# Performance work log

Hardware: AMD Instinct MI355X
Metric: run time of the kernel (lower is better)

## Reference

```python
import jax, jax.numpy as jnp
import numpy as np

B, A = 1024, 256                 # batch, padded action-space size
N_ENT, N_REL = 100000, 500
E_DIM, R_DIM, H_DIM = 200, 200, 400
ACT_DIM = E_DIM + R_DIM          # action embedding = [rel_emb ; ent_emb]
IN_DIM = E_DIM + H_DIM + R_DIM   # X = cat([E, H, Q])
HUGE = 1e31                      # ops.HUGE_INT
EPS = 1e-20


def setup_inputs() -> dict:
    key = jax.random.key(0)
    ks = jax.random.split(key, 12)
    inp = {
        "e": jax.random.randint(ks[0], (B,), 0, N_ENT),
        "q": jax.random.randint(ks[1], (B,), 0, N_REL),
        "H": jax.random.normal(ks[2], (B, H_DIM), dtype=jnp.float32),
        "r_space": jax.random.randint(ks[3], (B, A), 0, N_REL),
        "e_space": jax.random.randint(ks[4], (B, A), 0, N_ENT),
        "action_mask": jax.random.randint(ks[5], (B, A), 0, 2).astype(jnp.int32),
        # learned parameters
        "entity_emb": jax.random.normal(ks[6], (N_ENT, E_DIM), dtype=jnp.float32) * 0.02,
        "relation_emb": jax.random.normal(ks[7], (N_REL, R_DIM), dtype=jnp.float32) * 0.02,
        "W1": jax.random.normal(ks[8], (IN_DIM, ACT_DIM), dtype=jnp.float32) * (1.0 / np.sqrt(IN_DIM)),
        "b1": jnp.zeros((ACT_DIM,), jnp.float32),
        "W2": jax.random.normal(ks[9], (ACT_DIM, ACT_DIM), dtype=jnp.float32) * (1.0 / np.sqrt(ACT_DIM)),
        "b2": jnp.zeros((ACT_DIM,), jnp.float32),
        "W_att": jax.random.normal(ks[10], (ACT_DIM, R_DIM), dtype=jnp.float32) * (1.0 / np.sqrt(ACT_DIM)),
        "b_att": jnp.zeros((R_DIM,), jnp.float32),
    }
    return inp


def reference(e, q, H, r_space, e_space, action_mask,
              entity_emb, relation_emb, W1, b1, W2, b2, W_att, b_att):
    # state featurization: X = cat([E, H, Q])  -> [B, IN_DIM]
    E = entity_emb[e]
    Q = relation_emb[q]
    X = jnp.concatenate([E, H, Q], axis=-1)
    X = jax.nn.relu(X @ W1 + b1)          # W1 + ReLU (dropout = identity in eval)
    X2 = X @ W2 + b2                      # [B, ACT_DIM]

    # relation attention over all relations
    relation_att = jax.nn.softmax((X2 @ W_att + b_att) @ relation_emb.T, axis=-1)  # [B, N_REL]

    # action embeddings: A = cat([rel_emb[r_space], ent_emb[e_space]])  [B, A, ACT_DIM]
    A_emb = jnp.concatenate([relation_emb[r_space], entity_emb[e_space]], axis=-1)

    mask = action_mask.astype(X2.dtype)
    scores = jnp.einsum('bad,bd->ba', A_emb, X2) - (1.0 - mask) * HUGE
    action_dist = jax.nn.softmax(scores, axis=-1)                      # [B, A]
    entropy = -jnp.sum(action_dist * jnp.log(action_dist + EPS), axis=-1)  # [B]
    return action_dist, entropy, relation_att
```

## Files before the change

kernel.cpp:

```cpp
#include <hip/hip_runtime.h>

#define BATCH   1024
#define ASZ     256
#define EDIM    200
#define RDIM    200
#define HDIM    400
#define ACTDIM  400
#define INDIM   800
#define NRELS   500

typedef __attribute__((ext_vector_type(8))) short short8v;
typedef __attribute__((ext_vector_type(4))) float float4v;
typedef unsigned short u16;

__device__ __forceinline__ u16 f2bf(float f) {
    union { float f; unsigned u; } v; v.f = f;
    unsigned r = v.u + 0x7FFFu + ((v.u >> 16) & 1u);
    return (u16)(r >> 16);
}

template<int ABF, int BBF, int CT, int GAT, int RELU>
__device__ __forceinline__ void mgemm_body(
    const void* __restrict__ A, const void* __restrict__ B,
    float* __restrict__ Cp, u16* __restrict__ CTout, int ldct,
    const float* __restrict__ bias, float* __restrict__ Cf, u16* __restrict__ Cb,
    int M, int N, int K, int bn, int bm, int z, int nz,
    const int* e_s, const int* q_s,
    const float* __restrict__ Hm, const float* __restrict__ ent,
    const float* __restrict__ rel,
    short* As, short* Bs, int t)
{
    const int tot = (K + 31) >> 5;
    const int s0 = (z * tot) / nz, s1 = ((z + 1) * tot) / nz;

    const int lane = t & 63, w = t >> 6;
    const int l15 = lane & 15, l4 = lane >> 4;
    const int wr = (w >> 1) * 32, wc = (w & 1) * 32;

    const int row = t >> 2;
    const int kc  = (t & 3) * 8;

    auto loadA = [&](int s) -> uint4 {
        const int gk = (s << 5) + kc;
        __attribute__((aligned(16))) u16 v[8];
        if (GAT) {
            const float* p;
            if (gk < EDIM)              p = ent + (long)e_s[row] * EDIM + gk;
            else if (gk < EDIM + HDIM)  p = Hm  + (long)(bm + row) * HDIM + (gk - EDIM);
            else                        p = rel + (long)q_s[row] * RDIM + (gk - EDIM - HDIM);
            float4 f0 = *(const float4*)p;
            float4 f1 = *(const float4*)(p + 4);
            v[0]=f2bf(f0.x); v[1]=f2bf(f0.y); v[2]=f2bf(f0.z); v[3]=f2bf(f0.w);
            v[4]=f2bf(f1.x); v[5]=f2bf(f1.y); v[6]=f2bf(f1.z); v[7]=f2bf(f1.w);
            return *(uint4*)v;
        }
        const int gr = bm + row;
        if (gr < M && gk + 8 <= K) {
            if (ABF) return *(const uint4*)((const u16*)A + (long)gr * K + gk);
            const float* p = (const float*)A + (long)gr * K + gk;
            float4 f0 = *(const float4*)p;
            float4 f1 = *(const float4*)(p + 4);
            v[0]=f2bf(f0.x); v[1]=f2bf(f0.y); v[2]=f2bf(f0.z); v[3]=f2bf(f0.w);
            v[4]=f2bf(f1.x); v[5]=f2bf(f1.y); v[6]=f2bf(f1.z); v[7]=f2bf(f1.w);
            return *(uint4*)v;
        }
#pragma unroll
        for (int i = 0; i < 8; ++i) v[i] = 0;
        return *(uint4*)v;
    };
    auto loadB = [&](int s) -> uint4 {
        const int gk = (s << 5) + kc;
        const int gr = bn + row;
        __attribute__((aligned(16))) u16 v[8];
        if (gr < N && gk + 8 <= K) {
            if (BBF) return *(const uint4*)((const u16*)B + (long)gr * K + gk);
            const float* p = (const float*)B + (long)gr * K + gk;
            float4 f0 = *(const float4*)p;
            float4 f1 = *(const float4*)(p + 4);
            v[0]=f2bf(f0.x); v[1]=f2bf(f0.y); v[2]=f2bf(f0.z); v[3]=f2bf(f0.w);
            v[4]=f2bf(f1.x); v[5]=f2bf(f1.y); v[6]=f2bf(f1.z); v[7]=f2bf(f1.w);
            return *(uint4*)v;
        }
#pragma unroll
        for (int i = 0; i < 8; ++i) v[i] = 0;
        return *(uint4*)v;
    };

    float4v acc00 = {0.f,0.f,0.f,0.f}, acc01 = {0.f,0.f,0.f,0.f};
    float4v acc10 = {0.f,0.f,0.f,0.f}, acc11 = {0.f,0.f,0.f,0.f};

    uint4 ra = loadA(s0);
    uint4 rb = loadB(s0);

    for (int s = s0; s < s1; ++s) {
        *(uint4*)&As[row * 40 + kc] = ra;
        *(uint4*)&Bs[row * 40 + kc] = rb;
        __syncthreads();
        if (s + 1 < s1) {
            ra = loadA(s + 1);
            rb = loadB(s + 1);
        }
        short8v a0 = *(short8v*)&As[(wr      + l15) * 40 + l4 * 8];
        short8v a1 = *(short8v*)&As[(wr + 16 + l15) * 40 + l4 * 8];
        short8v b0 = *(short8v*)&Bs[(wc      + l15) * 40 + l4 * 8];
        short8v b1 = *(short8v*)&Bs[(wc + 16 + l15) * 40 + l4 * 8];
        acc00 = __builtin_amdgcn_mfma_f32_16x16x32_bf16(a0, b0, acc00, 0, 0, 0);
        acc01 = __builtin_amdgcn_mfma_f32_16x16x32_bf16(a0, b1, acc01, 0, 0, 0);
        acc10 = __builtin_amdgcn_mfma_f32_16x16x32_bf16(a1, b0, acc10, 0, 0, 0);
        acc11 = __builtin_amdgcn_mfma_f32_16x16x32_bf16(a1, b1, acc11, 0, 0, 0);
        __syncthreads();
    }

    const int rm0 = bm + wr + l4 * 4;
    const int cn0 = bn + wc + l15;
    if (CT == 1) {
        float* dst = Cp + (long)z * M * N;
#pragma unroll
        for (int r = 0; r < 4; ++r) {
            int gm0 = rm0 + r, gm1 = rm0 + 16 + r;
            if (gm0 < M) {
                if (cn0 < N)      dst[(long)gm0 * N + cn0]      = acc00[r];
                if (cn0 + 16 < N) dst[(long)gm0 * N + cn0 + 16] = acc01[r];
            }
            if (gm1 < M) {
                if (cn0 < N)      dst[(long)gm1 * N + cn0]      = acc10[r];
                if (cn0 + 16 < N) dst[(long)gm1 * N + cn0 + 16] = acc11[r];
            }
        }
    } else if (CT == 2) {
#pragma unroll
        for (int r = 0; r < 4; ++r) {
            int gm0 = rm0 + r, gm1 = rm0 + 16 + r;
            if (gm0 < M) {
                if (cn0 < N)      CTout[(long)cn0 * ldct + gm0]        = f2bf(acc00[r]);
                if (cn0 + 16 < N) CTout[(long)(cn0 + 16) * ldct + gm0] = f2bf(acc01[r]);
            }
            if (gm1 < M) {
                if (cn0 < N)      CTout[(long)cn0 * ldct + gm1]        = f2bf(acc10[r]);
                if (cn0 + 16 < N) CTout[(long)(cn0 + 16) * ldct + gm1] = f2bf(acc11[r]);
            }
        }
    } else {
        float bv0 = (cn0 < N)      ? bias[cn0]      : 0.f;
        float bv1 = (cn0 + 16 < N) ? bias[cn0 + 16] : 0.f;
#pragma unroll
        for (int r = 0; r < 4; ++r) {
            int gm0 = rm0 + r, gm1 = rm0 + 16 + r;
            if (gm0 < M) {
                if (cn0 < N) {
                    float v = acc00[r] + bv0;
                    if (RELU) v = fmaxf(v, 0.f);
                    Cf[(long)gm0 * N + cn0] = v;
                    Cb[(long)gm0 * N + cn0] = f2bf(v);
                }
                if (cn0 + 16 < N) {
                    float v = acc01[r] + bv1;
                    if (RELU) v = fmaxf(v, 0.f);
                    Cf[(long)gm0 * N + cn0 + 16] = v;
                    Cb[(long)gm0 * N + cn0 + 16] = f2bf(v);
                }
            }
            if (gm1 < M) {
                if (cn0 < N) {
                    float v = acc10[r] + bv0;
                    if (RELU) v = fmaxf(v, 0.f);
                    Cf[(long)gm1 * N + cn0] = v;
                    Cb[(long)gm1 * N + cn0] = f2bf(v);
                }
                if (cn0 + 16 < N) {
                    float v = acc11[r] + bv1;
                    if (RELU) v = fmaxf(v, 0.f);
                    Cf[(long)gm1 * N + cn0 + 16] = v;
                    Cb[(long)gm1 * N + cn0 + 16] = f2bf(v);
                }
            }
        }
    }
}

template<int ABF, int BBF, int CT, int GAT, int RELU>
__global__ __launch_bounds__(256) void k_mgemm(
    const void* __restrict__ A, const void* __restrict__ B,
    float* __restrict__ Cp, u16* __restrict__ CTout, int ldct,
    const float* __restrict__ bias, float* __restrict__ Cf, u16* __restrict__ Cb,
    int M, int N, int K,
    const int* __restrict__ eidx, const int* __restrict__ qidx,
    const float* __restrict__ Hm, const float* __restrict__ ent,
    const float* __restrict__ rel)
{
    __shared__ __align__(16) short As[64 * 40];
    __shared__ __align__(16) short Bs[64 * 40];
    __shared__ int e_s[64], q_s[64];
    const int t = threadIdx.x;
    const int bm = blockIdx.y * 64;
    if (GAT) {
        if (t < 64) {
            e_s[t] = eidx[bm + t];
            q_s[t] = qidx[bm + t];
        }
        __syncthreads();
    }
    mgemm_body<ABF, BBF, CT, GAT, RELU>(A, B, Cp, CTout, ldct, bias, Cf, Cb,
                                        M, N, K, blockIdx.x * 64, bm,
                                        blockIdx.z, gridDim.z,
                                        e_s, q_s, Hm, ent, rel, As, Bs, t);
}

__global__ __launch_bounds__(256) void k_prep_all(
    const float* __restrict__ W1, const float* __restrict__ W2,
    const float* __restrict__ batt, const float* __restrict__ rel,
    const float* __restrict__ Watt,
    u16* __restrict__ W1t, u16* __restrict__ W2t,
    u16* __restrict__ BbigT, float* __restrict__ bbig2)
{
    __shared__ __align__(16) short As[64 * 40];
    __shared__ __align__(16) short Bs[64 * 40];
    __shared__ float tile[32][33];
    __shared__ float bs[200];

    int blk = blockIdx.x, t = threadIdx.x;

    if (blk < 325) {
        int tk = blk / 13, tn = blk % 13;
        int k0 = tk * 32, n0 = tn * 32;
        int i = t >> 3, j4 = (t & 7) * 4;
#pragma unroll
        for (int jj = 0; jj < 4; ++jj) {
            int n = n0 + j4 + jj;
            tile[i][j4 + jj] = (n < 400) ? W1[(long)(k0 + i) * 400 + n] : 0.f;
        }
        __syncthreads();
        int o = t >> 3;
        if (n0 + o < 400) {
            ushort4 u;
            u.x = f2bf(tile[j4 + 0][o]); u.y = f2bf(tile[j4 + 1][o]);
            u.z = f2bf(tile[j4 + 2][o]); u.w = f2bf(tile[j4 + 3][o]);
            *(ushort4*)(W1t + (long)(n0 + o) * 800 + k0 + j4) = u;
        }
    } else if (blk < 494) {
        int idx = blk - 325;
        int tk = idx / 13, tn = idx % 13;
        int k0 = tk * 32, n0 = tn * 32;
        int i = t >> 3, j4 = (t & 7) * 4;
#pragma unroll
        for (int jj = 0; jj < 4; ++jj) {
            int n = n0 + j4 + jj;
            tile[i][j4 + jj] = (k0 + i < 400 && n < 400) ? W2[(long)(k0 + i) * 400 + n] : 0.f;
        }
        __syncthreads();
        int o = t >> 3;
        if (n0 + o < 400) {
#pragma unroll
            for (int jj = 0; jj < 4; ++jj) {
                int k = k0 + j4 + jj;
                if (k < 400) W2t[(long)(n0 + o) * 400 + k] = f2bf(tile[j4 + jj][o]);
            }
        }
    } else if (blk < 594) {
        int gid = (blk - 494) * 256 + t;
        for (int g = gid; g < 50000; g += 100 * 256) {
            int n = g / 100, kq = (g % 100) * 4;
            ushort4 u;
            u.x = (kq + 0 < 200) ? f2bf(rel[(long)n * 200 + kq + 0]) : (u16)0;
            u.y = (kq + 1 < 200) ? f2bf(rel[(long)n * 200 + kq + 1]) : (u16)0;
            u.z = (kq + 2 < 200) ? f2bf(rel[(long)n * 200 + kq + 2]) : (u16)0;
            u.w = (kq + 3 < 200) ? f2bf(rel[(long)n * 200 + kq + 3]) : (u16)0;
            *(ushort4*)(BbigT + (long)(500 + n) * 400 + kq) = u;
        }
    } else if (blk == 594) {
        if (t < 200) bs[t] = batt[t];
        __syncthreads();
        for (int n = t; n < NRELS; n += 256) {
            const float* rr = rel + (long)n * RDIM;
            float s = 0.f;
            for (int k = 0; k < 200; ++k) s += bs[k] * rr[k];
            bbig2[n] = s;
        }
    } else {
        int idx = blk - 595;
        int bn = (idx & 7) * 64, bm = (idx >> 3) * 64;
        mgemm_body<0, 0, 2, 0, 0>(Watt, rel, nullptr, BbigT, 400,
                                  nullptr, nullptr, nullptr,
                                  400, 500, 200, bn, bm, 0, 1,
                                  nullptr, nullptr, nullptr, nullptr, nullptr,
                                  As, Bs, t);
    }
}

template<int RELU, int OUT>
__global__ __launch_bounds__(128) void k_reduce2(
    const float* __restrict__ Cp, const float* __restrict__ bias,
    float* __restrict__ Cf, u16* __restrict__ Cb, int M, int N, int nks)
{
    int m = blockIdx.x;
    int nf4 = N >> 2;
    for (int f = threadIdx.x; f < nf4; f += 128) {
        long off = (long)m * N + f * 4;
        float4 s = *(const float4*)(Cp + off);
        for (int ks = 1; ks < nks; ++ks) {
            float4 v = *(const float4*)(Cp + (long)ks * M * N + off);
            s.x += v.x; s.y += v.y; s.z += v.z; s.w += v.w;
        }
        float4 bb = *(const float4*)(bias + f * 4);
        s.x += bb.x; s.y += bb.y; s.z += bb.z; s.w += bb.w;
        if (RELU) {
            s.x = fmaxf(s.x, 0.f); s.y = fmaxf(s.y, 0.f);
            s.z = fmaxf(s.z, 0.f); s.w = fmaxf(s.w, 0.f);
        }
        if (OUT != 1) *(float4*)(Cf + off) = s;
        if (OUT != 0) {
            ushort4 u;
            u.x = f2bf(s.x); u.y = f2bf(s.y); u.z = f2bf(s.z); u.w = f2bf(s.w);
            *(ushort4*)(Cb + off) = u;
        }
    }
}

__global__ __launch_bounds__(512) void k_scores(
    const float* __restrict__ X2, const float* __restrict__ Cp,
    const float* __restrict__ brel,
    const int* __restrict__ r_space, const int* __restrict__ e_space,
    const int* __restrict__ amask,
    const float* __restrict__ ent_emb,
    float* __restrict__ out_dist, float* __restrict__ out_ent,
    float* __restrict__ out_rel)
{
    int b = blockIdx.x, t = threadIdx.x;
    int wave = t >> 6, lane = t & 63;
    __shared__ __align__(16) float4 xt4[50];
    __shared__ float xr[NRELS];
    __shared__ float sc[ASZ];
    __shared__ int   smask[ASZ];
    __shared__ float red[8];

    const float* rowX2 = X2 + (long)b * ACTDIM;
    const float* c0 = Cp + (long)b * 1000;
    const float* c1 = Cp + (long)BATCH * 1000 + (long)b * 1000;
    if (t < 50) xt4[t] = *(const float4*)(rowX2 + 200 + 4 * t);
    for (int i = t; i < NRELS; i += 512) xr[i] = c0[500 + i] + c1[500 + i];

    int abase = wave * 32;
    int r_idx = 0, e_idx = 0, mk = 0;
    if (lane < 32) {
        long base = (long)b * ASZ + abase + lane;
        r_idx = r_space[base];
        e_idx = e_space[base];
        mk    = amask[base];
        smask[abase + lane] = mk;
    }
    __syncthreads();

    float4 x = (lane < 50) ? xt4[lane] : make_float4(0.f, 0.f, 0.f, 0.f);
    const int g = lane >> 4;

#pragma unroll
    for (int i = 0; i < 4; ++i) {
        float s[8] = {0.f,0.f,0.f,0.f,0.f,0.f,0.f,0.f};
        int rj[8];
#pragma unroll
        for (int j = 0; j < 8; ++j) {
            int a = 8 * i + j;
            int m0 = __shfl(mk, a);
            rj[j]  = __shfl(r_idx, a);
            if (m0) {
                int e0 = __shfl(e_idx, a);
                if (lane < 50) {
                    float4 v = ((const float4*)(ent_emb + (long)e0 * EDIM))[lane];
                    s[j] = fmaf(v.x, x.x, fmaf(v.y, x.y, fmaf(v.z, x.z, v.w * x.w)));
                }
            }
        }
#pragma unroll
        for (int j = 0; j < 8; ++j) {
            s[j] += __shfl_xor(s[j], 32);
            s[j] += __shfl_xor(s[j], 16);
        }
        float v0 = (g == 0) ? s[0] : (g == 1) ? s[1] : (g == 2) ? s[2] : s[3];
        float v1 = (g == 0) ? s[4] : (g == 1) ? s[5] : (g == 2) ? s[6] : s[7];
#pragma unroll
        for (int off = 8; off > 0; off >>= 1) {
            v0 += __shfl_xor(v0, off);
            v1 += __shfl_xor(v1, off);
        }
        int r0sel = (g == 0) ? rj[0] : (g == 1) ? rj[1] : (g == 2) ? rj[2] : rj[3];
        int r1sel = (g == 0) ? rj[4] : (g == 1) ? rj[5] : (g == 2) ? rj[6] : rj[7];
        if ((lane & 15) == 0) {
            sc[abase + 8 * i + g]     = v0 + xr[r0sel];
            sc[abase + 8 * i + 4 + g] = v1 + xr[r1sel];
        }
    }
    __syncthreads();

    float v = -3.4e38f;
    float evv = 0.f;
    if (t < ASZ) v = smask[t] ? sc[t] : -1e31f;

    float m = v;
#pragma unroll
    for (int off = 32; off > 0; off >>= 1) m = fmaxf(m, __shfl_xor(m, off));
    if (t < ASZ && lane == 0) red[wave] = m;
    __syncthreads();
    float mm = fmaxf(fmaxf(red[0], red[1]), fmaxf(red[2], red[3]));
    __syncthreads();

    if (t < ASZ) evv = expf(v - mm);
    float ss = evv;
#pragma unroll
    for (int off = 32; off > 0; off >>= 1) ss += __shfl_xor(ss, off);
    if (t < ASZ && lane == 0) red[wave] = ss;
    __syncthreads();
    float tot = red[0] + red[1] + red[2] + red[3];
    __syncthreads();

    float term = 0.f;
    if (t < ASZ) {
        float p = evv / tot;
        out_dist[(long)b * ASZ + t] = p;
        term = p * logf(p + 1e-20f);
    }
#pragma unroll
    for (int off = 32; off > 0; off >>= 1) term += __shfl_xor(term, off);
    if (t < ASZ && lane == 0) red[wave] = term;
    __syncthreads();
    if (t == 0) out_ent[b] = -(red[0] + red[1] + red[2] + red[3]);
    __syncthreads();

    float rv = (t < NRELS) ? (c0[t] + c1[t] + brel[t]) : -3.4e38f;

    float rm = rv;
#pragma unroll
    for (int off = 32; off > 0; off >>= 1) rm = fmaxf(rm, __shfl_xor(rm, off));
    if (lane == 0) red[wave] = rm;
    __syncthreads();
    rm = fmaxf(fmaxf(fmaxf(red[0], red[1]), fmaxf(red[2], red[3])),
               fmaxf(fmaxf(red[4], red[5]), fmaxf(red[6], red[7])));
    __syncthreads();

    float rev = (t < NRELS) ? expf(rv - rm) : 0.f;
    float rs = rev;
#pragma unroll
    for (int off = 32; off > 0; off >>= 1) rs += __shfl_xor(rs, off);
    if (lane == 0) red[wave] = rs;
    __syncthreads();
    rs = red[0] + red[1] + red[2] + red[3] + red[4] + red[5] + red[6] + red[7];
    if (t < NRELS) out_rel[(long)b * NRELS + t] = rev / rs;
}

extern "C" void kernel_launch(void* const* d_in, const int* in_sizes, int n_in,
                              void* d_out, int out_size, void* d_ws, size_t ws_size,
                              hipStream_t stream)
{
    const int*   e       = (const int*)  d_in[0];
    const int*   q       = (const int*)  d_in[1];
    const float* H       = (const float*)d_in[2];
    const int*   r_space = (const int*)  d_in[3];
    const int*   e_space = (const int*)  d_in[4];
    const int*   amask   = (const int*)  d_in[5];
    const float* ent     = (const float*)d_in[6];
    const float* rel     = (const float*)d_in[7];
    const float* W1      = (const float*)d_in[8];
    const float* b1      = (const float*)d_in[9];
    const float* W2      = (const float*)d_in[10];
    const float* b2      = (const float*)d_in[11];
    const float* Watt    = (const float*)d_in[12];
    const float* batt    = (const float*)d_in[13];

    float* out      = (float*)d_out;
    float* out_dist = out;
    float* out_ent  = out + (long)BATCH * ASZ;
    float* out_rel  = out_ent + BATCH;

    char* ws = (char*)d_ws;
    u16*   X1_bf  = (u16*)  (ws + 0);
    float* X2     = (float*)(ws + 819200);
    u16*   X2_bf  = (u16*)  (ws + 2457600);
    u16*   W1t    = (u16*)  (ws + 3276800);
    u16*   W2t    = (u16*)  (ws + 3916800);
    u16*   BbigT  = (u16*)  (ws + 4236800);
    float* bbig2  = (float*)(ws + 5036800);
    float* Cp     = (float*)(ws + 5242880);

    k_prep_all<<<651, 256, 0, stream>>>(W1, W2, batt, rel, Watt,
                                        W1t, W2t, BbigT, bbig2);

    k_mgemm<1, 1, 1, 1, 0><<<dim3(7, 16, 4), 256, 0, stream>>>(
        nullptr, W1t, Cp, nullptr, 0, nullptr, nullptr, nullptr,
        BATCH, ACTDIM, INDIM, e, q, H, ent, rel);
    k_reduce2<1, 1><<<BATCH, 128, 0, stream>>>(Cp, b1, nullptr, X1_bf, BATCH, ACTDIM, 4);

    k_mgemm<1, 1, 3, 0, 0><<<dim3(7, 16, 1), 256, 0, stream>>>(
        X1_bf, W2t, nullptr, nullptr, 0, b2, X2, X2_bf,
        BATCH, ACTDIM, ACTDIM, nullptr, nullptr, nullptr, nullptr, nullptr);

    k_mgemm<1, 1, 1, 0, 0><<<dim3(16, 16, 2), 256, 0, stream>>>(
        X2_bf, BbigT, Cp, nullptr, 0, nullptr, nullptr, nullptr,
        BATCH, 1000, ACTDIM, nullptr, nullptr, nullptr, nullptr, nullptr);

    k_scores<<<BATCH, 512, 0, stream>>>(X2, Cp, bbig2, r_space, e_space, amask,
                                        ent, out_dist, out_ent, out_rel);
}
```

Before: 80.48 us.

## Fuse split-K reduction into next GEMM load and drop split-K on relation GEMM

```diff
diff --git a/kernel.cpp b/kernel.cpp
--- a/kernel.cpp
+++ b/kernel.cpp
@@ -22,6 +22,7 @@
 template<int ABF, int BBF, int CT, int GAT, int RELU>
 __device__ __forceinline__ void mgemm_body(
     const void* __restrict__ A, const void* __restrict__ B,
+    const float* __restrict__ biasA,
     float* __restrict__ Cp, u16* __restrict__ CTout, int ldct,
     const float* __restrict__ bias, float* __restrict__ Cf, u16* __restrict__ Cb,
     int M, int N, int K, int bn, int bm, int z, int nz,
@@ -55,8 +56,29 @@
             return *(uint4*)v;
         }
         const int gr = bm + row;
+        if (ABF == 2) {
+            const long sl = (long)M * K;
+            const float* p0 = (const float*)A + (long)gr * K + gk;
+            float4 a0 = *(const float4*)p0,        a1 = *(const float4*)(p0 + 4);
+            float4 b0 = *(const float4*)(p0 + sl), b1 = *(const float4*)(p0 + sl + 4);
+            float4 c0 = *(const float4*)(p0+2*sl), c1 = *(const float4*)(p0 + 2*sl + 4);
+            float4 d0 = *(const float4*)(p0+3*sl), d1 = *(const float4*)(p0 + 3*sl + 4);
+            float4 e0 = *(const float4*)(biasA + gk);
+            float4 e1 = *(const float4*)(biasA + gk + 4);
+            float s0v = fmaxf(a0.x + b0.x + c0.x + d0.x + e0.x, 0.f);
+            float s1v = fmaxf(a0.y + b0.y + c0.y + d0.y + e0.y, 0.f);
+            float s2v = fmaxf(a0.z + b0.z + c0.z + d0.z + e0.z, 0.f);
+            float s3v = fmaxf(a0.w + b0.w + c0.w + d0.w + e0.w, 0.f);
+            float s4v = fmaxf(a1.x + b1.x + c1.x + d1.x + e1.x, 0.f);
+            float s5v = fmaxf(a1.y + b1.y + c1.y + d1.y + e1.y, 0.f);
+            float s6v = fmaxf(a1.z + b1.z + c1.z + d1.z + e1.z, 0.f);
+            float s7v = fmaxf(a1.w + b1.w + c1.w + d1.w + e1.w, 0.f);
+            v[0]=f2bf(s0v); v[1]=f2bf(s1v); v[2]=f2bf(s2v); v[3]=f2bf(s3v);
+            v[4]=f2bf(s4v); v[5]=f2bf(s5v); v[6]=f2bf(s6v); v[7]=f2bf(s7v);
+            return *(uint4*)v;
+        }
         if (gr < M && gk + 8 <= K) {
-            if (ABF) return *(const uint4*)((const u16*)A + (long)gr * K + gk);
+            if (ABF == 1) return *(const uint4*)((const u16*)A + (long)gr * K + gk);
             const float* p = (const float*)A + (long)gr * K + gk;
             float4 f0 = *(const float4*)p;
             float4 f1 = *(const float4*)(p + 4);
@@ -140,7 +162,7 @@
                 if (cn0 + 16 < N) CTout[(long)(cn0 + 16) * ldct + gm1] = f2bf(acc11[r]);
             }
         }
-    } else {
+    } else if (CT == 3) {
         float bv0 = (cn0 < N)      ? bias[cn0]      : 0.f;
         float bv1 = (cn0 + 16 < N) ? bias[cn0 + 16] : 0.f;
 #pragma unroll
@@ -175,12 +197,28 @@
                 }
             }
         }
+    } else {
+        float bv0 = (cn0 < N)      ? bias[cn0]      : 0.f;
+        float bv1 = (cn0 + 16 < N) ? bias[cn0 + 16] : 0.f;
+#pragma unroll
+        for (int r = 0; r < 4; ++r) {
+            int gm0 = rm0 + r, gm1 = rm0 + 16 + r;
+            if (gm0 < M) {
+                if (cn0 < N)      Cf[(long)gm0 * N + cn0]      = acc00[r] + bv0;
+                if (cn0 + 16 < N) Cf[(long)gm0 * N + cn0 + 16] = acc01[r] + bv1;
+            }
+            if (gm1 < M) {
+                if (cn0 < N)      Cf[(long)gm1 * N + cn0]      = acc10[r] + bv0;
+                if (cn0 + 16 < N) Cf[(long)gm1 * N + cn0 + 16] = acc11[r] + bv1;
+            }
+        }
     }
 }
 
 template<int ABF, int BBF, int CT, int GAT, int RELU>
 __global__ __launch_bounds__(256) void k_mgemm(
     const void* __restrict__ A, const void* __restrict__ B,
+    const float* __restrict__ biasA,
     float* __restrict__ Cp, u16* __restrict__ CTout, int ldct,
     const float* __restrict__ bias, float* __restrict__ Cf, u16* __restrict__ Cb,
     int M, int N, int K,
@@ -200,7 +238,7 @@
         }
         __syncthreads();
     }
-    mgemm_body<ABF, BBF, CT, GAT, RELU>(A, B, Cp, CTout, ldct, bias, Cf, Cb,
+    mgemm_body<ABF, BBF, CT, GAT, RELU>(A, B, biasA, Cp, CTout, ldct, bias, Cf, Cb,
                                         M, N, K, blockIdx.x * 64, bm,
                                         blockIdx.z, gridDim.z,
                                         e_s, q_s, Hm, ent, rel, As, Bs, t);
@@ -211,7 +249,7 @@
     const float* __restrict__ batt, const float* __restrict__ rel,
     const float* __restrict__ Watt,
     u16* __restrict__ W1t, u16* __restrict__ W2t,
-    u16* __restrict__ BbigT, float* __restrict__ bbig2)
+    u16* __restrict__ BbigT, float* __restrict__ bbig3)
 {
     __shared__ __align__(16) short As[64 * 40];
     __shared__ __align__(16) short Bs[64 * 40];
@@ -274,12 +312,13 @@
             const float* rr = rel + (long)n * RDIM;
             float s = 0.f;
             for (int k = 0; k < 200; ++k) s += bs[k] * rr[k];
-            bbig2[n] = s;
-        }
+            bbig3[n] = s;
+        }
+        for (int n = t; n < 500; n += 256) bbig3[500 + n] = 0.f;
     } else {
         int idx = blk - 595;
         int bn = (idx & 7) * 64, bm = (idx >> 3) * 64;
-        mgemm_body<0, 0, 2, 0, 0>(Watt, rel, nullptr, BbigT, 400,
+        mgemm_body<0, 0, 2, 0, 0>(Watt, rel, nullptr, nullptr, BbigT, 400,
                                   nullptr, nullptr, nullptr,
                                   400, 500, 200, bn, bm, 0, 1,
                                   nullptr, nullptr, nullptr, nullptr, nullptr,
@@ -287,38 +326,8 @@
     }
 }
 
-template<int RELU, int OUT>
-__global__ __launch_bounds__(128) void k_reduce2(
-    const float* __restrict__ Cp, const float* __restrict__ bias,
-    float* __restrict__ Cf, u16* __restrict__ Cb, int M, int N, int nks)
-{
-    int m = blockIdx.x;
-    int nf4 = N >> 2;
-    for (int f = threadIdx.x; f < nf4; f += 128) {
-        long off = (long)m * N + f * 4;
-        float4 s = *(const float4*)(Cp + off);
-        for (int ks = 1; ks < nks; ++ks) {
-            float4 v = *(const float4*)(Cp + (long)ks * M * N + off);
-            s.x += v.x; s.y += v.y; s.z += v.z; s.w += v.w;
-        }
-        float4 bb = *(const float4*)(bias + f * 4);
-        s.x += bb.x; s.y += bb.y; s.z += bb.z; s.w += bb.w;
-        if (RELU) {
-            s.x = fmaxf(s.x, 0.f); s.y = fmaxf(s.y, 0.f);
-            s.z = fmaxf(s.z, 0.f); s.w = fmaxf(s.w, 0.f);
-        }
-        if (OUT != 1) *(float4*)(Cf + off) = s;
-        if (OUT != 0) {
-            ushort4 u;
-            u.x = f2bf(s.x); u.y = f2bf(s.y); u.z = f2bf(s.z); u.w = f2bf(s.w);
-            *(ushort4*)(Cb + off) = u;
-        }
-    }
-}
-
 __global__ __launch_bounds__(512) void k_scores(
-    const float* __restrict__ X2, const float* __restrict__ Cp,
-    const float* __restrict__ brel,
+    const float* __restrict__ X2, const float* __restrict__ SX,
     const int* __restrict__ r_space, const int* __restrict__ e_space,
     const int* __restrict__ amask,
     const float* __restrict__ ent_emb,
@@ -334,10 +343,9 @@
     __shared__ float red[8];
 
     const float* rowX2 = X2 + (long)b * ACTDIM;
-    const float* c0 = Cp + (long)b * 1000;
-    const float* c1 = Cp + (long)BATCH * 1000 + (long)b * 1000;
+    const float* rowS  = SX + (long)b * 1000;
     if (t < 50) xt4[t] = *(const float4*)(rowX2 + 200 + 4 * t);
-    for (int i = t; i < NRELS; i += 512) xr[i] = c0[500 + i] + c1[500 + i];
+    for (int i = t; i < NRELS; i += 512) xr[i] = rowS[500 + i];
 
     int abase = wave * 32;
     int r_idx = 0, e_idx = 0, mk = 0;
@@ -425,7 +433,7 @@
     if (t == 0) out_ent[b] = -(red[0] + red[1] + red[2] + red[3]);
     __syncthreads();
 
-    float rv = (t < NRELS) ? (c0[t] + c1[t] + brel[t]) : -3.4e38f;
+    float rv = (t < NRELS) ? rowS[t] : -3.4e38f;
 
     float rm = rv;
 #pragma unroll
@@ -471,31 +479,30 @@
     float* out_rel  = out_ent + BATCH;
 
     char* ws = (char*)d_ws;
-    u16*   X1_bf  = (u16*)  (ws + 0);
-    float* X2     = (float*)(ws + 819200);
-    u16*   X2_bf  = (u16*)  (ws + 2457600);
-    u16*   W1t    = (u16*)  (ws + 3276800);
-    u16*   W2t    = (u16*)  (ws + 3916800);
-    u16*   BbigT  = (u16*)  (ws + 4236800);
-    float* bbig2  = (float*)(ws + 5036800);
-    float* Cp     = (float*)(ws + 5242880);
+    float* X2    = (float*)(ws + 0);
+    u16*   X2_bf = (u16*)  (ws + 1638400);
+    u16*   W1t   = (u16*)  (ws + 2457600);
+    u16*   W2t   = (u16*)  (ws + 3097600);
+    u16*   BbigT = (u16*)  (ws + 3417600);
+    float* bbig3 = (float*)(ws + 4217600);
+    float* SX    = (float*)(ws + 4221600);
+    float* Cp    = (float*)(ws + 8317600);
 
     k_prep_all<<<651, 256, 0, stream>>>(W1, W2, batt, rel, Watt,
-                                        W1t, W2t, BbigT, bbig2);
+                                        W1t, W2t, BbigT, bbig3);
 
     k_mgemm<1, 1, 1, 1, 0><<<dim3(7, 16, 4), 256, 0, stream>>>(
-        nullptr, W1t, Cp, nullptr, 0, nullptr, nullptr, nullptr,
+        nullptr, W1t, nullptr, Cp, nullptr, 0, nullptr, nullptr, nullptr,
         BATCH, ACTDIM, INDIM, e, q, H, ent, rel);
-    k_reduce2<1, 1><<<BATCH, 128, 0, stream>>>(Cp, b1, nullptr, X1_bf, BATCH, ACTDIM, 4);
-
-    k_mgemm<1, 1, 3, 0, 0><<<dim3(7, 16, 1), 256, 0, stream>>>(
-        X1_bf, W2t, nullptr, nullptr, 0, b2, X2, X2_bf,
+
+    k_mgemm<2, 1, 3, 0, 0><<<dim3(7, 16, 1), 256, 0, stream>>>(
+        Cp, W2t, b1, nullptr, nullptr, 0, b2, X2, X2_bf,
         BATCH, ACTDIM, ACTDIM, nullptr, nullptr, nullptr, nullptr, nullptr);
 
-    k_mgemm<1, 1, 1, 0, 0><<<dim3(16, 16, 2), 256, 0, stream>>>(
-        X2_bf, BbigT, Cp, nullptr, 0, nullptr, nullptr, nullptr,
+    k_mgemm<1, 1, 4, 0, 0><<<dim3(16, 16, 1), 256, 0, stream>>>(
+        X2_bf, BbigT, nullptr, nullptr, nullptr, 0, bbig3, SX, nullptr,
         BATCH, 1000, ACTDIM, nullptr, nullptr, nullptr, nullptr, nullptr);
 
-    k_scores<<<BATCH, 512, 0, stream>>>(X2, Cp, bbig2, r_space, e_space, amask,
+    k_scores<<<BATCH, 512, 0, stream>>>(X2, SX, r_space, e_space, amask,
                                         ent, out_dist, out_ent, out_rel);
 }
```

Result: slower. 90.47 us (+12.4%).
